# Performance work log

Measured on AMD Instinct MI355X. Metric: run time of the kernel, lower is better.

Reference implementation:

```python
import jax, jax.numpy as jnp
import numpy as np

B, S, H, E, V, NSTEPS = 8, 128, 512, 512, 32000, 8


def setup_inputs() -> dict:
    key = jax.random.key(0)
    ks = jax.random.split(key, 24)

    def lin(k, fi, fo):
        return (jax.random.normal(k, (fi, fo), jnp.float32) / np.sqrt(fi).astype(np.float32))

    return {
        "input_ids": jax.random.randint(ks[0], (B, S), 0, V),
        "tree_ids": jax.random.randint(ks[1], (B, NSTEPS, 3, S), 0, S),
        "emb": jax.random.normal(ks[2], (V, E), jnp.float32) * 0.02,
        "W_ioux": lin(ks[3], E, 3 * H),
        "W_iouh_r": lin(ks[4], H, 3 * H),
        "b_iouh_r": jnp.zeros((3 * H,), jnp.float32),
        "W_iouh_l": lin(ks[5], H, 3 * H),
        "b_iouh_l": jnp.zeros((3 * H,), jnp.float32),
        "W_fx": lin(ks[6], E, H),
        "W_fh0": lin(ks[7], H, H),
        "b_fh0": jnp.zeros((H,), jnp.float32),
        "W_fh1": lin(ks[8], H, H),
        "b_fh1": jnp.zeros((H,), jnp.float32),
        "W_fh2": lin(ks[9], H, H),
        "b_fh2": jnp.zeros((H,), jnp.float32),
        "W_fh3": lin(ks[10], H, H),
        "b_fh3": jnp.zeros((H,), jnp.float32),
    }


def _scatter_rows(vals, idx):
    # out[b, idx[b, j], k] += vals[b, j, k]  (torch scatter_add_ along dim 1)
    return jax.vmap(lambda v, i: jnp.zeros_like(v).at[i].add(v))(vals, idx)


def _gather_rows(vals, idx):
    # out[b, j, k] = vals[b, idx[b, j], k]  (torch gather along dim 1)
    return jnp.take_along_axis(vals, idx[:, :, None], axis=1)


def _masked_scatter(dest, mask_rows, src):
    # Exact torch masked_scatter_ semantics: flatten mask/src, fill True slots
    # with consecutive elements of flattened src.
    m = jnp.broadcast_to(mask_rows[:, :, None], dest.shape).reshape(-1)
    pos = jnp.clip(jnp.cumsum(m) - 1, 0, None)
    out = jnp.where(m, src.reshape(-1)[pos], dest.reshape(-1))
    return out.reshape(dest.shape)


def reference(input_ids, tree_ids, emb, W_ioux, W_iouh_r, b_iouh_r, W_iouh_l,
              b_iouh_l, W_fx, W_fh0, b_fh0, W_fh1, b_fh1, W_fh2, b_fh2,
              W_fh3, b_fh3):
    x = emb[input_ids]                      # [B, S, E]
    Hs = W_fx.shape[1]
    iou_x = x @ W_ioux                      # [B, S, 3H], loop-invariant
    fx_x = x @ W_fx                         # [B, S, H],  loop-invariant
    h0 = jnp.zeros(x.shape[:2] + (Hs,), x.dtype)
    c0 = jnp.zeros_like(h0)
    steps = jnp.transpose(tree_ids, (1, 0, 2, 3))  # [n_steps, B, 3, S]

    def step(carry, t):
        h, c = carry
        idx_d, idx_r, idx_l = t[:, 0], t[:, 1], t[:, 2]
        iou_hr = h @ W_iouh_r + b_iouh_r
        iou_hl = h @ W_iouh_l + b_iouh_l
        # torch scatter_add_ with an index of width H into a 3H buffer only
        # touches the first H channels -- replicate that exactly.
        scat = _scatter_rows(iou_hr[..., :Hs], idx_r) + _scatter_rows(iou_hl[..., :Hs], idx_l)
        iou = iou_x.at[..., :Hs].add(scat)
        i, o, u = jnp.split(iou, 3, axis=-1)
        i, o, u = jax.nn.sigmoid(i), jax.nn.sigmoid(o), jnp.tanh(u)
        # fh0 and fh1 share idx_r, fh2 and fh3 share idx_l -> fold linearly.
        fh_r = h @ (W_fh0 + W_fh1) + (b_fh0 + b_fh1)
        fh_l = h @ (W_fh2 + W_fh3) + (b_fh2 + b_fh3)
        f = jax.nn.sigmoid(_gather_rows(fx_x, idx_d)
                           + _gather_rows(fh_r, idx_r)
                           + _gather_rows(fh_l, idx_l))
        fc = f * c
        c_full = i * u + _scatter_rows(fc, idx_d)
        h_full = o * jnp.tanh(c_full)
        mask = idx_d != 0
        h_new = _masked_scatter(h, mask, h_full)
        c_new = _masked_scatter(c, mask, c_full)
        return (h_new, c_new), None

    (h, c), _ = jax.lax.scan(step, (h0, c0), steps)
    return h
```

## Files before the change

### kernel.cpp

```cpp
#include <hip/hip_runtime.h>
#include <hip/hip_bf16.h>

#define B_ 8
#define S_ 128
#define H_ 512
#define E_ 512
#define NST 8
#define R_ 1024
#define N2 2048
#define KD 512
#define LDA 72

typedef __hip_bfloat16 bf16;
typedef __attribute__((ext_vector_type(8))) short v8s;
typedef __attribute__((ext_vector_type(4))) float v4f;

__device__ __forceinline__ float sigm(float x){ return 1.0f/(1.0f + expf(-x)); }
__device__ __forceinline__ float load_in(const void* p, long long i, int isb){
    return isb ? __bfloat162float(((const bf16*)p)[i]) : ((const float*)p)[i];
}
__device__ __forceinline__ int idx_read(const int* p, int j, int is64){
    return is64 ? p[2*j] : p[j];
}
__device__ __forceinline__ unsigned short f2b(float v){
    bf16 b = __float2bfloat16(v);
    return *(unsigned short*)&b;
}

__global__ void probe_all(const void* t0, const void* t1, const void* t2, const void* t3,
                          const void* t4, const void* t5, const void* t6, const void* t7,
                          const void* t8, const void* t9, const void* t10, const void* t11,
                          const void* t12, const void* t13, const void* t14,
                          const int* __restrict__ ids, const int* __restrict__ tree,
                          int* __restrict__ flags){
    const void* ts[15] = {t0,t1,t2,t3,t4,t5,t6,t7,t8,t9,t10,t11,t12,t13,t14};
    int bid = blockIdx.x, t = threadIdx.x;
    int bad = 0;
    if (bid < 15){
        if (t < 512){
            unsigned short u = ((const unsigned short*)ts[bid])[t];
            bad = (((u >> 7) & 0xFF) >= 140);
        }
    } else {
        const int* p = (bid == 15) ? ids : tree;
        int n = (bid == 15) ? 1024 : 2048;
        for (int j = t; j < n; j += 1024)
            if (j & 1) bad |= (p[j] != 0);
    }
    unsigned long long bl = __ballot(bad);
    __shared__ int acc[16];
    if ((t & 63) == 0) acc[t >> 6] = (bl != 0ull) ? 1 : 0;
    __syncthreads();
    if (t == 0){
        int any = 0;
        for (int w = 0; w < 16; ++w) any |= acc[w];
        flags[(bid < 15) ? bid : (16 + bid - 15)] = any ? 0 : 1;
    }
}

#define NB2 320
#define GS2 (NB2*512)
__global__ __launch_bounds__(512)
void rank_pack(const void* __restrict__ Wioux, const void* __restrict__ Wfx,
               const void* __restrict__ Wr, const void* __restrict__ Wl,
               const void* __restrict__ W0, const void* __restrict__ W1,
               const void* __restrict__ W2, const void* __restrict__ W3,
               const void* __restrict__ br, const void* __restrict__ bl,
               const void* __restrict__ b0, const void* __restrict__ b1,
               const void* __restrict__ b2, const void* __restrict__ b3,
               const int* __restrict__ ids, const void* __restrict__ emb,
               const int* __restrict__ tree,
               unsigned short* __restrict__ WxT, unsigned short* __restrict__ WcatT,
               float* __restrict__ bcat, unsigned short* __restrict__ xb,
               float* __restrict__ h0,
               int* __restrict__ msk, int* __restrict__ rnk, int* __restrict__ cnt,
               const int* __restrict__ flags){
    int bid = blockIdx.x, tid = threadIdx.x;
    int is64 = flags[17];
    if (bid < 8){
        int st = bid;
        for (int c = tid; c < R_; c += 512){
            cnt[(0*NST + st)*R_ + c] = 0;
            cnt[(1*NST + st)*R_ + c] = 0;
            cnt[(2*NST + st)*R_ + c] = 0;
        }
        __syncthreads();
        __shared__ int wt[8];
        int runbase = 0;
        for (int ch = 0; ch < 2; ++ch){
            int t = ch*512 + tid;
            int b = t >> 7, s = t & 127;
            int base = (b*NST + st)*3*S_;
            int d0 = idx_read(tree, base + s, is64);
            int rd = (b<<7) + d0;
            int rr = (b<<7) + idx_read(tree, base + S_ + s, is64);
            int rl = (b<<7) + idx_read(tree, base + 2*S_ + s, is64);
            int m = (d0 != 0) ? 1 : 0;
            unsigned long long bal = __ballot(m);
            int lane = tid & 63, wv = tid >> 6;
            if (lane == 0) wt[wv] = __popcll(bal);
            __syncthreads();
            int bp = runbase, tot = 0;
            for (int w = 0; w < wv; ++w) bp += wt[w];
            for (int w = 0; w < 8; ++w) tot += wt[w];
            int rank = bp + __popcll(bal & ((1ull << lane) - 1ull));
            msk[st*R_ + t] = m;
            rnk[st*R_ + t] = m ? rank : 0;
            atomicAdd(&cnt[(0*NST + st)*R_ + rr], 1);
            atomicAdd(&cnt[(1*NST + st)*R_ + rl], 1);
            atomicAdd(&cnt[(2*NST + st)*R_ + rd], 1);
            runbase += tot;
            __syncthreads();
        }
    }
    int gt = bid*512 + tid;
    {
        int f_wx = flags[1], f_wf = flags[6];
        for (int u = gt; u < 131072; u += GS2){
            int n = u >> 6, k0 = (u & 63)*8;
            unsigned short tmp[8];
            #pragma unroll
            for (int i = 0; i < 8; ++i){
                float v = (n < 1536) ? load_in(Wioux, (long long)(k0+i)*1536 + n, f_wx)
                                     : load_in(Wfx,   (long long)(k0+i)*512 + (n-1536), f_wf);
                tmp[i] = f2b(v);
            }
            *(v8s*)&WxT[(size_t)n*KD + k0] = *(v8s*)tmp;
        }
    }
    {
        int fWr=flags[2], fWl=flags[4], fW0=flags[7], fW1=flags[9], fW2=flags[11], fW3=flags[13];
        for (int u = gt; u < 131072; u += GS2){
            int n = u >> 6, k0 = (u & 63)*8;
            unsigned short tmp[8];
            #pragma unroll
            for (int i = 0; i < 8; ++i){
                long long k = k0 + i;
                float v;
                if      (n <  512) v = load_in(Wr, k*1536 + n, fWr);
                else if (n < 1024) v = load_in(Wl, k*1536 + (n-512), fWl);
                else if (n < 1536) { int c = n-1024; v = load_in(W0, k*512+c, fW0) + load_in(W1, k*512+c, fW1); }
                else               { int c = n-1536; v = load_in(W2, k*512+c, fW2) + load_in(W3, k*512+c, fW3); }
                tmp[i] = f2b(v);
            }
            *(v8s*)&WcatT[(size_t)n*KD + k0] = *(v8s*)tmp;
        }
    }
    {
        int fbr=flags[3], fbl=flags[5], fb0=flags[8], fb1=flags[10], fb2=flags[12], fb3=flags[14];
        for (int n = gt; n < 2048; n += GS2){
            float v;
            if      (n <  512) v = load_in(br, n, fbr);
            else if (n < 1024) v = load_in(bl, n-512, fbl);
            else if (n < 1536) v = load_in(b0, n-1024, fb0) + load_in(b1, n-1024, fb1);
            else               v = load_in(b2, n-1536, fb2) + load_in(b3, n-1536, fb3);
            bcat[n] = v;
        }
    }
    {
        int f_emb = flags[0], i64i = flags[16];
        for (int u = gt; u < 65536; u += GS2){
            int r = u >> 6, c0 = (u & 63)*8;
            long long base = (long long)idx_read(ids, r, i64i)*E_ + c0;
            unsigned short tmp[8];
            #pragma unroll
            for (int i = 0; i < 8; ++i) tmp[i] = f2b(load_in(emb, base + i, f_emb));
            *(v8s*)&xb[(size_t)r*KD + c0] = *(v8s*)tmp;
        }
    }
    for (int u = gt; u < 262144; u += GS2)
        ((float4*)h0)[u] = make_float4(0.f,0.f,0.f,0.f);
}

__global__ void csr_scan(const int* __restrict__ cnt, int* __restrict__ off,
                         int* __restrict__ cur){
    int st = blockIdx.x, a = blockIdx.y;
    int t = threadIdx.x;
    int base = (a*NST + st)*R_;
    __shared__ int sh[R_];
    int v = cnt[base + t];
    sh[t] = v;
    __syncthreads();
    for (int d = 1; d < R_; d <<= 1){
        int x = (t >= d) ? sh[t - d] : 0;
        __syncthreads();
        sh[t] += x;
        __syncthreads();
    }
    int excl = sh[t] - v;
    off[base + t] = excl;
    cur[base + t] = excl;
}

__global__ __launch_bounds__(512)
void csr_fill(const int* __restrict__ tree, int* __restrict__ cur,
              int* __restrict__ ent, const int* __restrict__ flags){
    int is64 = flags[17];
    int st = blockIdx.x;
    for (int ch = 0; ch < 2; ++ch){
        int t = ch*512 + threadIdx.x;
        int b = t >> 7, s = t & 127;
        int base = (b*NST + st)*3*S_;
        int rd = (b<<7) + idx_read(tree, base + s, is64);
        int rr = (b<<7) + idx_read(tree, base + S_ + s, is64);
        int rl = (b<<7) + idx_read(tree, base + 2*S_ + s, is64);
        int p0 = atomicAdd(&cur[(0*NST + st)*R_ + rr], 1);
        ent[(0*NST + st)*R_ + p0] = t;
        int p1 = atomicAdd(&cur[(1*NST + st)*R_ + rl], 1);
        ent[(1*NST + st)*R_ + p1] = t;
        int p2 = atomicAdd(&cur[(2*NST + st)*R_ + rd], 1);
        ent[(2*NST + st)*R_ + p2] = t | (rr << 10) | (rl << 20);
    }
}

__global__ __launch_bounds__(256)
void gemm_bf16(const unsigned short* __restrict__ A,
               const unsigned short* __restrict__ BT,
               const float* __restrict__ bias,
               float* __restrict__ C){
    __shared__ short As[64*LDA];
    __shared__ short Bs[64*LDA];
    int bn = blockIdx.x, bm = blockIdx.y;
    int tid = threadIdx.x;
    int lane = tid & 63, wave = tid >> 6;
    int wm = wave & 1, wn = wave >> 1;
    int lm = lane & 15, quad = lane >> 4;
    v4f acc[2][2];
    #pragma unroll
    for (int i=0;i<2;++i)
        #pragma unroll
        for (int j=0;j<2;++j) acc[i][j] = (v4f)0.0f;

    int srow = tid >> 3, sg = (tid & 7)*8;
    const unsigned short* Ab = A  + (size_t)(bm*64)*KD;
    const unsigned short* Bb = BT + (size_t)(bn*64)*KD;
    v8s pa[2], pb[2];
    #pragma unroll
    for (int j=0;j<2;++j){
        pa[j] = *(const v8s*)(Ab + (size_t)(j*32+srow)*KD + sg);
        pb[j] = *(const v8s*)(Bb + (size_t)(j*32+srow)*KD + sg);
    }
    for (int k0 = 0; k0 < KD; k0 += 64){
        #pragma unroll
        for (int j=0;j<2;++j){
            *(v8s*)&As[(j*32+srow)*LDA + sg] = pa[j];
            *(v8s*)&Bs[(j*32+srow)*LDA + sg] = pb[j];
        }
        __syncthreads();
        int k1 = k0 + 64;
        if (k1 < KD){
            #pragma unroll
            for (int j=0;j<2;++j){
                pa[j] = *(const v8s*)(Ab + (size_t)(j*32+srow)*KD + k1 + sg);
                pb[j] = *(const v8s*)(Bb + (size_t)(j*32+srow)*KD + k1 + sg);
            }
        }
        #pragma unroll
        for (int kk = 0; kk < 64; kk += 32){
            v8s af[2], bf[2];
            #pragma unroll
            for (int i=0;i<2;++i){
                af[i] = *(const v8s*)&As[(wm*32 + i*16 + lm)*LDA + kk + quad*8];
                bf[i] = *(const v8s*)&Bs[(wn*32 + i*16 + lm)*LDA + kk + quad*8];
            }
            #pragma unroll
            for (int i=0;i<2;++i)
                #pragma unroll
                for (int j=0;j<2;++j)
                    acc[i][j] = __builtin_amdgcn_mfma_f32_16x16x32_bf16(af[i], bf[j], acc[i][j], 0, 0, 0);
        }
        __syncthreads();
    }
    #pragma unroll
    for (int j=0;j<2;++j){
        int n = bn*64 + wn*32 + j*16 + lm;
        float bv = bias ? bias[n] : 0.0f;
        #pragma unroll
        for (int i=0;i<2;++i){
            int m0 = bm*64 + wm*32 + i*16 + quad*4;
            #pragma unroll
            for (int rg = 0; rg < 4; ++rg)
                C[(size_t)(m0+rg)*N2 + n] = acc[i][j][rg] + bv;
        }
    }
}

__global__ __launch_bounds__(512)
void step_epi(const float* __restrict__ XO, const float* __restrict__ T, int tstr,
              const float* __restrict__ hc, const float* __restrict__ cc,
              float* __restrict__ hn, float* __restrict__ cn,
              unsigned short* __restrict__ hb, float* __restrict__ out,
              const int* __restrict__ msk, const int* __restrict__ rnk,
              const int* __restrict__ cnt, const int* __restrict__ off,
              const int* __restrict__ ent, int st, int last){
    int r = blockIdx.x, c = threadIdx.x;
    if (!msk[st*R_ + r]){
        float hv = hc[(size_t)r*H_ + c];
        if (last){ out[(size_t)r*H_ + c] = hv; return; }
        hn[(size_t)r*H_ + c] = hv;
        cn[(size_t)r*H_ + c] = cc[(size_t)r*H_ + c];
        hb[(size_t)r*KD + c] = f2b(hv);
        return;
    }
    int j = rnk[st*R_ + r];
    int bR = off[(0*NST+st)*R_ + j], dR = cnt[(0*NST+st)*R_ + j];
    int bL = off[(1*NST+st)*R_ + j], dL = cnt[(1*NST+st)*R_ + j];
    int bD = off[(2*NST+st)*R_ + j], dD = cnt[(2*NST+st)*R_ + j];
    const int* eR = ent + (0*NST+st)*R_ + bR;
    const int* eL = ent + (1*NST+st)*R_ + bL;
    const int* eD = ent + (2*NST+st)*R_ + bD;
    const float* xo = XO + (size_t)j*N2;
    float scv = 0.f;
    for (int e = 0; e < dR; ++e) scv += T[(size_t)eR[e]*tstr + c];
    for (int e = 0; e < dL; ++e) scv += T[(size_t)eL[e]*tstr + 512 + c];
    float fxv = xo[1536 + c];
    float csc = 0.f;
    for (int e = 0; e < dD; ++e){
        int pk = eD[e];
        int s  = pk & 1023, rr = (pk >> 10) & 1023, rl = (pk >> 20) & 1023;
        float f = sigm(fxv + T[(size_t)rr*tstr + 1024 + c] + T[(size_t)rl*tstr + 1536 + c]);
        csc += f * cc[(size_t)s*H_ + c];
    }
    float ig = sigm(xo[c] + scv);
    float og = sigm(xo[512 + c]);
    float ug = tanhf(xo[1024 + c]);
    float cf = ig*ug + csc;
    float hf = og * tanhf(cf);
    if (last){ out[(size_t)r*H_ + c] = hf; return; }
    hn[(size_t)r*H_ + c] = hf;
    cn[(size_t)r*H_ + c] = cf;
    hb[(size_t)r*KD + c] = f2b(hf);
}

extern "C" void kernel_launch(void* const* d_in, const int* in_sizes, int n_in,
                              void* d_out, int out_size, void* d_ws, size_t ws_size,
                              hipStream_t stream) {
    const int* input_ids = (const int*)d_in[0];
    const int* tree      = (const int*)d_in[1];

    char* wp = (char*)d_ws;
    auto alloc = [&](size_t bytes) -> void* {
        void* q = (void*)wp;
        wp += (bytes + 255) & ~(size_t)255;
        return q;
    };
    float*          XO     = (float*)alloc((size_t)R_*N2*4);
    float*          T      = (float*)alloc((size_t)R_*N2*4);
    float*          h0     = (float*)alloc((size_t)R_*H_*4);
    float*          c0     = (float*)alloc((size_t)R_*H_*4);
    float*          h1     = (float*)alloc((size_t)R_*H_*4);
    float*          c1     = (float*)alloc((size_t)R_*H_*4);
    unsigned short* WxT    = (unsigned short*)alloc((size_t)N2*KD*2);
    unsigned short* WcatT  = (unsigned short*)alloc((size_t)N2*KD*2);
    float*          bcat   = (float*)alloc((size_t)N2*4);
    unsigned short* xb     = (unsigned short*)alloc((size_t)R_*KD*2);
    unsigned short* hb     = (unsigned short*)alloc((size_t)R_*KD*2);
    int*            msk    = (int*)alloc((size_t)NST*R_*4);
    int*            rnk    = (int*)alloc((size_t)NST*R_*4);
    int*            cnt    = (int*)alloc((size_t)3*NST*R_*4);
    int*            off    = (int*)alloc((size_t)3*NST*R_*4);
    int*            cur    = (int*)alloc((size_t)3*NST*R_*4);
    int*            ent    = (int*)alloc((size_t)3*NST*R_*4);
    int*            flags  = (int*)alloc(256);
    float*          out    = (float*)d_out;

    hipLaunchKernelGGL(probe_all, dim3(17), dim3(1024), 0, stream,
                       d_in[2], d_in[3], d_in[4], d_in[5], d_in[6], d_in[7], d_in[8],
                       d_in[9], d_in[10], d_in[11], d_in[12], d_in[13], d_in[14],
                       d_in[15], d_in[16], input_ids, tree, flags);
    hipLaunchKernelGGL(rank_pack, dim3(NB2), dim3(512), 0, stream,
                       d_in[3], d_in[8],
                       d_in[4], d_in[6], d_in[9], d_in[11], d_in[13], d_in[15],
                       d_in[5], d_in[7], d_in[10], d_in[12], d_in[14], d_in[16],
                       input_ids, d_in[2], tree,
                       WxT, WcatT, bcat, xb, h0, msk, rnk, cnt, flags);
    hipLaunchKernelGGL(csr_scan, dim3(NST, 3), dim3(1024), 0, stream, cnt, off, cur);
    hipLaunchKernelGGL(csr_fill, dim3(NST), dim3(512), 0, stream, tree, cur, ent, flags);

    hipLaunchKernelGGL(gemm_bf16, dim3(N2/64, R_/64), dim3(256), 0, stream,
                       xb, WxT, (const float*)nullptr, XO);

    float *hc = h0, *cc = c0, *hn = h1, *cn = c1;
    hipLaunchKernelGGL(step_epi, dim3(R_), dim3(512), 0, stream,
                       XO, bcat, 0, hc, cc, hn, cn, hb, out,
                       msk, rnk, cnt, off, ent, 0, 0);
    { float* t1 = hc; hc = hn; hn = t1; float* t2 = cc; cc = cn; cn = t2; }

    for (int st = 1; st < NST; ++st){
        hipLaunchKernelGGL(gemm_bf16, dim3(N2/64, R_/64), dim3(256), 0, stream,
                           hb, WcatT, bcat, T);
        hipLaunchKernelGGL(step_epi, dim3(R_), dim3(512), 0, stream,
                           XO, T, N2, hc, cc, hn, cn, hb, out,
                           msk, rnk, cnt, off, ent, st, (st == NST-1) ? 1 : 0);
        float* t1 = hc; hc = hn; hn = t1;
        float* t2 = cc; cc = cn; cn = t2;
    }
}
```

Baseline: 287.9 us.

## Fuse per-step GEMM and epilogue launches into one persistent kernel with grid barriers

Replaces the 16 alternating gemm_bf16/step_epi launches with a single persistent kernel of 512 blocks. The blocks step through the GEMM and epilogue phases, separated by a software grid barrier built on an atomic counter in global memory. The epilogue now handles two rows per 256-thread block, and the GEMM tile index is remapped from a 1D block id. This removes kernel launch gaps, at the cost of spin-wait barriers and reliance on all 512 blocks being co-resident (launch_bounds 256,2). If they are not all resident, the kernel can deadlock.

```diff
diff --git a/kernel.cpp b/kernel.cpp
--- a/kernel.cpp
+++ b/kernel.cpp
@@ -10,6 +10,7 @@
 #define N2 2048
 #define KD 512
 #define LDA 72
+#define NBLK 512
 
 typedef __hip_bfloat16 bf16;
 typedef __attribute__((ext_vector_type(8))) short v8s;
@@ -25,6 +26,18 @@
 __device__ __forceinline__ unsigned short f2b(float v){
     bf16 b = __float2bfloat16(v);
     return *(unsigned short*)&b;
+}
+
+__device__ __forceinline__ void gsync(int* bar, int target){
+    __syncthreads();
+    if (threadIdx.x == 0){
+        __threadfence();
+        __hip_atomic_fetch_add(bar, 1, __ATOMIC_RELAXED, __HIP_MEMORY_SCOPE_AGENT);
+        while (__hip_atomic_load(bar, __ATOMIC_RELAXED, __HIP_MEMORY_SCOPE_AGENT) < target)
+            __builtin_amdgcn_s_sleep(2);
+        __threadfence();
+    }
+    __syncthreads();
 }
 
 __global__ void probe_all(const void* t0, const void* t1, const void* t2, const void* t3,
@@ -74,9 +87,10 @@
                float* __restrict__ bcat, unsigned short* __restrict__ xb,
                float* __restrict__ h0,
                int* __restrict__ msk, int* __restrict__ rnk, int* __restrict__ cnt,
-               const int* __restrict__ flags){
+               const int* __restrict__ flags, int* __restrict__ bar){
     int bid = blockIdx.x, tid = threadIdx.x;
     int is64 = flags[17];
+    if (bid == 0 && tid == 0) *bar = 0;
     if (bid < 8){
         int st = bid;
         for (int c = tid; c < R_; c += 512){
@@ -213,14 +227,15 @@
     }
 }
 
-__global__ __launch_bounds__(256)
-void gemm_bf16(const unsigned short* __restrict__ A,
+__device__ __forceinline__ void gemm_phase(const unsigned short* __restrict__ A,
                const unsigned short* __restrict__ BT,
                const float* __restrict__ bias,
-               float* __restrict__ C){
-    __shared__ short As[64*LDA];
-    __shared__ short Bs[64*LDA];
-    int bn = blockIdx.x, bm = blockIdx.y;
+               float* __restrict__ C,
+               short* __restrict__ As, short* __restrict__ Bs)
+{
+    int bid = blockIdx.x;
+    int bn = (bid & 7)*4 + ((bid >> 3) & 3);
+    int bm = bid >> 5;
     int tid = threadIdx.x;
     int lane = tid & 63, wave = tid >> 6;
     int wm = wave & 1, wn = wave >> 1;
@@ -285,51 +300,113 @@
     }
 }
 
-__global__ __launch_bounds__(512)
-void step_epi(const float* __restrict__ XO, const float* __restrict__ T, int tstr,
+__device__ __forceinline__ void epi_phase(const float* __restrict__ XO,
+              const float* __restrict__ T, int tstr,
               const float* __restrict__ hc, const float* __restrict__ cc,
               float* __restrict__ hn, float* __restrict__ cn,
               unsigned short* __restrict__ hb, float* __restrict__ out,
               const int* __restrict__ msk, const int* __restrict__ rnk,
               const int* __restrict__ cnt, const int* __restrict__ off,
-              const int* __restrict__ ent, int st, int last){
-    int r = blockIdx.x, c = threadIdx.x;
-    if (!msk[st*R_ + r]){
-        float hv = hc[(size_t)r*H_ + c];
-        if (last){ out[(size_t)r*H_ + c] = hv; return; }
-        hn[(size_t)r*H_ + c] = hv;
-        cn[(size_t)r*H_ + c] = cc[(size_t)r*H_ + c];
-        hb[(size_t)r*KD + c] = f2b(hv);
-        return;
-    }
-    int j = rnk[st*R_ + r];
-    int bR = off[(0*NST+st)*R_ + j], dR = cnt[(0*NST+st)*R_ + j];
-    int bL = off[(1*NST+st)*R_ + j], dL = cnt[(1*NST+st)*R_ + j];
-    int bD = off[(2*NST+st)*R_ + j], dD = cnt[(2*NST+st)*R_ + j];
-    const int* eR = ent + (0*NST+st)*R_ + bR;
-    const int* eL = ent + (1*NST+st)*R_ + bL;
-    const int* eD = ent + (2*NST+st)*R_ + bD;
-    const float* xo = XO + (size_t)j*N2;
-    float scv = 0.f;
-    for (int e = 0; e < dR; ++e) scv += T[(size_t)eR[e]*tstr + c];
-    for (int e = 0; e < dL; ++e) scv += T[(size_t)eL[e]*tstr + 512 + c];
-    float fxv = xo[1536 + c];
-    float csc = 0.f;
-    for (int e = 0; e < dD; ++e){
-        int pk = eD[e];
-        int s  = pk & 1023, rr = (pk >> 10) & 1023, rl = (pk >> 20) & 1023;
-        float f = sigm(fxv + T[(size_t)rr*tstr + 1024 + c] + T[(size_t)rl*tstr + 1536 + c]);
-        csc += f * cc[(size_t)s*H_ + c];
-    }
-    float ig = sigm(xo[c] + scv);
-    float og = sigm(xo[512 + c]);
-    float ug = tanhf(xo[1024 + c]);
-    float cf = ig*ug + csc;
-    float hf = og * tanhf(cf);
-    if (last){ out[(size_t)r*H_ + c] = hf; return; }
-    hn[(size_t)r*H_ + c] = hf;
-    cn[(size_t)r*H_ + c] = cf;
-    hb[(size_t)r*KD + c] = f2b(hf);
+              const int* __restrict__ ent, int st, int last)
+{
+    int tid = threadIdx.x;
+    int c0 = tid, c1 = tid + 256;
+    #pragma unroll
+    for (int rr2 = 0; rr2 < 2; ++rr2){
+        int r = blockIdx.x*2 + rr2;
+        if (!msk[st*R_ + r]){
+            float hv0 = hc[(size_t)r*H_ + c0];
+            float hv1 = hc[(size_t)r*H_ + c1];
+            if (last){
+                out[(size_t)r*H_ + c0] = hv0;
+                out[(size_t)r*H_ + c1] = hv1;
+            } else {
+                hn[(size_t)r*H_ + c0] = hv0;
+                hn[(size_t)r*H_ + c1] = hv1;
+                cn[(size_t)r*H_ + c0] = cc[(size_t)r*H_ + c0];
+                cn[(size_t)r*H_ + c1] = cc[(size_t)r*H_ + c1];
+                hb[(size_t)r*KD + c0] = f2b(hv0);
+                hb[(size_t)r*KD + c1] = f2b(hv1);
+            }
+            continue;
+        }
+        int j = rnk[st*R_ + r];
+        int bR = off[(0*NST+st)*R_ + j], dR = cnt[(0*NST+st)*R_ + j];
+        int bL = off[(1*NST+st)*R_ + j], dL = cnt[(1*NST+st)*R_ + j];
+        int bD = off[(2*NST+st)*R_ + j], dD = cnt[(2*NST+st)*R_ + j];
+        const int* eR = ent + (0*NST+st)*R_ + bR;
+        const int* eL = ent + (1*NST+st)*R_ + bL;
+        const int* eD = ent + (2*NST+st)*R_ + bD;
+        const float* xo = XO + (size_t)j*N2;
+        float scv0 = 0.f, scv1 = 0.f;
+        for (int e = 0; e < dR; ++e){
+            size_t b = (size_t)eR[e]*tstr;
+            scv0 += T[b + c0]; scv1 += T[b + c1];
+        }
+        for (int e = 0; e < dL; ++e){
+            size_t b = (size_t)eL[e]*tstr + 512;
+            scv0 += T[b + c0]; scv1 += T[b + c1];
+        }
+        float fx0 = xo[1536 + c0], fx1 = xo[1536 + c1];
+        float csc0 = 0.f, csc1 = 0.f;
+        for (int e = 0; e < dD; ++e){
+            int pk = eD[e];
+            int s  = pk & 1023, ra = (pk >> 10) & 1023, rb = (pk >> 20) & 1023;
+            size_t ba = (size_t)ra*tstr + 1024, bb = (size_t)rb*tstr + 1536;
+            float f0 = sigm(fx0 + T[ba + c0] + T[bb + c0]);
+            float f1 = sigm(fx1 + T[ba + c1] + T[bb + c1]);
+            csc0 += f0 * cc[(size_t)s*H_ + c0];
+            csc1 += f1 * cc[(size_t)s*H_ + c1];
+        }
+        float ig0 = sigm(xo[c0] + scv0), ig1 = sigm(xo[c1] + scv1);
+        float og0 = sigm(xo[512 + c0]), og1 = sigm(xo[512 + c1]);
+        float ug0 = tanhf(xo[1024 + c0]), ug1 = tanhf(xo[1024 + c1]);
+        float cf0 = ig0*ug0 + csc0, cf1 = ig1*ug1 + csc1;
+        float hf0 = og0 * tanhf(cf0), hf1 = og1 * tanhf(cf1);
+        if (last){
+            out[(size_t)r*H_ + c0] = hf0;
+            out[(size_t)r*H_ + c1] = hf1;
+        } else {
+            hn[(size_t)r*H_ + c0] = hf0; hn[(size_t)r*H_ + c1] = hf1;
+            cn[(size_t)r*H_ + c0] = cf0; cn[(size_t)r*H_ + c1] = cf1;
+            hb[(size_t)r*KD + c0] = f2b(hf0); hb[(size_t)r*KD + c1] = f2b(hf1);
+        }
+    }
+}
+
+__global__ __launch_bounds__(256, 2)
+void chain_all(const unsigned short* __restrict__ xb,
+               const unsigned short* __restrict__ WxT,
+               const unsigned short* __restrict__ WcatT,
+               const float* __restrict__ bcat,
+               float* __restrict__ XO, float* __restrict__ T,
+               float* __restrict__ h0, float* __restrict__ c0,
+               float* __restrict__ h1, float* __restrict__ c1,
+               unsigned short* __restrict__ hb, float* __restrict__ out,
+               const int* __restrict__ msk, const int* __restrict__ rnk,
+               const int* __restrict__ cnt, const int* __restrict__ off,
+               const int* __restrict__ ent, int* bar)
+{
+    __shared__ short As[64*LDA];
+    __shared__ short Bs[64*LDA];
+    int gen = 0;
+
+    gemm_phase(xb, WxT, (const float*)nullptr, XO, As, Bs);
+    gsync(bar, NBLK*(++gen));
+    epi_phase(XO, bcat, 0, h0, c0, h1, c1, hb, out, msk, rnk, cnt, off, ent, 0, 0);
+    gsync(bar, NBLK*(++gen));
+
+    for (int st = 1; st < NST; ++st){
+        const float* hcp = (st & 1) ? h1 : h0;
+        const float* ccp = (st & 1) ? c1 : c0;
+        float* hnp = (st & 1) ? h0 : h1;
+        float* cnp = (st & 1) ? c0 : c1;
+        gemm_phase(hb, WcatT, bcat, T, As, Bs);
+        gsync(bar, NBLK*(++gen));
+        epi_phase(XO, T, N2, hcp, ccp, hnp, cnp, hb, out,
+                  msk, rnk, cnt, off, ent, st, (st == NST-1) ? 1 : 0);
+        if (st < NST-1) gsync(bar, NBLK*(++gen));
+    }
 }
 
 extern "C" void kernel_launch(void* const* d_in, const int* in_sizes, int n_in,
@@ -362,6 +439,7 @@
     int*            cur    = (int*)alloc((size_t)3*NST*R_*4);
     int*            ent    = (int*)alloc((size_t)3*NST*R_*4);
     int*            flags  = (int*)alloc(256);
+    int*            bar    = (int*)alloc(256);
     float*          out    = (float*)d_out;
 
     hipLaunchKernelGGL(probe_all, dim3(17), dim3(1024), 0, stream,
@@ -373,26 +451,11 @@
                        d_in[4], d_in[6], d_in[9], d_in[11], d_in[13], d_in[15],
                        d_in[5], d_in[7], d_in[10], d_in[12], d_in[14], d_in[16],
                        input_ids, d_in[2], tree,
-                       WxT, WcatT, bcat, xb, h0, msk, rnk, cnt, flags);
+                       WxT, WcatT, bcat, xb, h0, msk, rnk, cnt, flags, bar);
     hipLaunchKernelGGL(csr_scan, dim3(NST, 3), dim3(1024), 0, stream, cnt, off, cur);
     hipLaunchKernelGGL(csr_fill, dim3(NST), dim3(512), 0, stream, tree, cur, ent, flags);
 
-    hipLaunchKernelGGL(gemm_bf16, dim3(N2/64, R_/64), dim3(256), 0, stream,
-                       xb, WxT, (const float*)nullptr, XO);
-
-    float *hc = h0, *cc = c0, *hn = h1, *cn = c1;
-    hipLaunchKernelGGL(step_epi, dim3(R_), dim3(512), 0, stream,
-                       XO, bcat, 0, hc, cc, hn, cn, hb, out,
-                       msk, rnk, cnt, off, ent, 0, 0);
-    { float* t1 = hc; hc = hn; hn = t1; float* t2 = cc; cc = cn; cn = t2; }
-
-    for (int st = 1; st < NST; ++st){
-        hipLaunchKernelGGL(gemm_bf16, dim3(N2/64, R_/64), dim3(256), 0, stream,
-                           hb, WcatT, bcat, T);
-        hipLaunchKernelGGL(step_epi, dim3(R_), dim3(512), 0, stream,
-                           XO, T, N2, hc, cc, hn, cn, hb, out,
-                           msk, rnk, cnt, off, ent, st, (st == NST-1) ? 1 : 0);
-        float* t1 = hc; hc = hn; hn = t1;
-        float* t2 = cc; cc = cn; cn = t2;
-    }
-}
+    hipLaunchKernelGGL(chain_all, dim3(NBLK), dim3(256), 0, stream,
+                       xb, WxT, WcatT, bcat, XO, T, h0, c0, h1, c1, hb, out,
+                       msk, rnk, cnt, off, ent, bar);
+}
```

Result: slower. 1.131 ms (+293.0%).
